# Kernel optimization log

Measured on AMD Instinct MI355X. Metric: run time of the kernel, lower is better.

The kernel has to match this reference:

```python
import jax, jax.numpy as jnp
import numpy as np

B, C, NUM_CLASSES = 16384, 4096, 64
BLOCK_LEN = 819          # round(4096 * 0.2)
N_BLOCKS = 1


def setup_inputs() -> dict:
    key = jax.random.key(0)
    kx, kw, ks = jax.random.split(key, 3)
    x = jax.random.normal(kx, (B, C), dtype=jnp.float32)
    W = jax.random.normal(kw, (NUM_CLASSES, C), dtype=jnp.float32) * 0.02
    b = jnp.zeros((NUM_CLASSES,), dtype=jnp.float32)
    # valid starts in [0, C - BLOCK_LEN], randint upper bound exclusive
    starts = jax.random.randint(ks, (B, N_BLOCKS), 0, C - BLOCK_LEN + 1, dtype=jnp.int32)
    return {"x": x, "W": W, "b": b, "starts": starts}


def reference(x, W, b, starts):
    # Vectorized DropBlock1D (training mode): zero a contiguous channel
    # segment of length BLOCK_LEN per sample per block, then Linear.
    pos = jnp.arange(C, dtype=jnp.int32)                      # [C]
    s = starts[:, :, None]                                    # [B, NB, 1]
    blocked = (pos[None, None, :] >= s) & (pos[None, None, :] < s + BLOCK_LEN)
    keep = ~jnp.any(blocked, axis=1)                           # [B, C]
    xm = x * keep.astype(x.dtype)                              # [B, C]
    return xm @ W.T + b                                        # [B, num_classes]
```

## Files before the change

### kernel.cpp

```cpp
#include <hip/hip_runtime.h>
#include <stdint.h>

#define BROWS 16384
#define CDIM  4096
#define NCLS  64
#define BLKLEN 819u
#define NWAVES 8
#define MROWS 32
#define CH 256
#define NCHUNK (CDIM / CH)

typedef __attribute__((ext_vector_type(4))) float f32x4;
typedef __attribute__((ext_vector_type(8))) short s16x8;

static __device__ __forceinline__ unsigned short f2bf(float f) {
    union { float f; unsigned u; } v; v.f = f;
    unsigned u = v.u;
    u += 0x7FFFu + ((u >> 16) & 1u);
    return (unsigned short)(u >> 16);
}

static __device__ __forceinline__ void gload_lds16(const void* g, void* l) {
    __builtin_amdgcn_global_load_lds(
        (const __attribute__((address_space(1))) unsigned int*)g,
        (__attribute__((address_space(3))) unsigned int*)l,
        16, 0, 0);
}

__global__ __launch_bounds__(256) void convert_w_fragmajor(const float* __restrict__ W,
                                                           unsigned short* __restrict__ Wfm) {
    const int u    = blockIdx.x * 256 + threadIdx.x;
    const int lane = u & 63;
    const int t    = (u >> 6) & 3;
    const int kk   = u >> 8;
    const int row  = t * 16 + (lane & 15);
    const int col  = kk * 32 + (lane >> 4) * 8;
    const float* p = W + (size_t)row * CDIM + col;
    f32x4 a = *reinterpret_cast<const f32x4*>(p);
    f32x4 b = *reinterpret_cast<const f32x4*>(p + 4);
    s16x8 o;
    #pragma unroll
    for (int j = 0; j < 4; ++j) {
        o[j]     = (short)f2bf(a[j]);
        o[j + 4] = (short)f2bf(b[j]);
    }
    *reinterpret_cast<s16x8*>(Wfm + (size_t)u * 8) = o;
}

template<bool PRECONV>
__global__ __launch_bounds__(512, 4) void dropblock_gemm_kernel(
    const float* __restrict__ x,
    const float* __restrict__ Wf,
    const unsigned short* __restrict__ Wfm,
    const float* __restrict__ bias,
    const int* __restrict__ starts,
    float* __restrict__ out)
{
    __shared__ float lds[NWAVES][2][MROWS][32];
    const int tid  = threadIdx.x;
    const int lane = tid & 63;
    const int wv   = tid >> 6;
    const int l16  = lane & 15;
    const int lg   = lane >> 4;
    const int row_base = blockIdx.x * MROWS;

    const int s0 = starts[row_base + l16];
    const int s1 = starts[row_base + 16 + l16];
    int sr[4];
    #pragma unroll
    for (int i = 0; i < 4; ++i) sr[i] = starts[row_base + i * 8 + (lane >> 3)];

    const unsigned swzA = (unsigned)((l16 & 7) << 4);
    char* mybuf = (char*)&lds[wv][0][0][0];

    f32x4 acc[2][4];
    #pragma unroll
    for (int f = 0; f < 2; ++f)
        #pragma unroll
        for (int t = 0; t < 4; ++t) acc[f][t] = (f32x4){0.f, 0.f, 0.f, 0.f};

    auto stage = [&](int ch, int b) {
        char* lb = mybuf + b * 4096;
        const size_t colbase = (size_t)ch * CH + (size_t)wv * 32;
        const char* gclamp = (const char*)x + ((size_t)row_base * CDIM + colbase) * 4;
        #pragma unroll
        for (int i = 0; i < 4; ++i) {
            const int r = i * 8 + (lane >> 3);
            const unsigned wb = ((unsigned)((lane & 7) * 16)) ^ ((unsigned)((r & 7) << 4));
            const int c0 = (int)colbase + (int)(wb >> 2);
            const bool fullmask = (unsigned)(c0 - sr[i]) <= (BLKLEN - 4u);
            const char* gnorm = (const char*)x
                + ((size_t)(row_base + r) * CDIM + colbase) * 4 + wb;
            const char* g = fullmask ? gclamp : gnorm;
            gload_lds16(g, lb + i * 1024);
        }
    };

    s16x8 wfr[2][4];
    auto loadW = [&](int ch, int b) {
        const int kk = ch * 8 + wv;
        #pragma unroll
        for (int t = 0; t < 4; ++t)
            wfr[b][t] = *reinterpret_cast<const s16x8*>(
                Wfm + ((size_t)((kk * 4 + t) * 64 + lane)) * 8);
    };

    stage(0, 0);
    if (PRECONV) loadW(0, 0);

    #pragma unroll
    for (int ch = 0; ch < NCHUNK; ++ch) {
        const int b = ch & 1;

        if (ch + 1 < NCHUNK) {
            if (PRECONV) loadW(ch + 1, b ^ 1);
            stage(ch + 1, b ^ 1);
        }

        __builtin_amdgcn_sched_barrier(0);
        if (ch + 1 < NCHUNK) {
            if (PRECONV) asm volatile("s_waitcnt vmcnt(8)" ::: "memory");
            else         asm volatile("s_waitcnt vmcnt(4)" ::: "memory");
        } else {
            asm volatile("s_waitcnt vmcnt(0)" ::: "memory");
        }
        __builtin_amdgcn_sched_barrier(0);

        const char* lb = mybuf + b * 4096;
        #pragma unroll
        for (int f = 0; f < 2; ++f) {
            const int row = f * 16 + l16;
            const unsigned a0 = (unsigned)(row * 128 + lg * 32);
            f32x4 xa = *reinterpret_cast<const f32x4*>(lb + (a0 ^ swzA));
            f32x4 xb = *reinterpret_cast<const f32x4*>(lb + ((a0 + 16) ^ swzA));

            const int d0 = ch * CH + wv * 32 + lg * 8 - (f ? s1 : s0);
            s16x8 afrag;
            #pragma unroll
            for (int j = 0; j < 4; ++j) {
                float va = ((unsigned)(d0 + j)     >= BLKLEN) ? xa[j] : 0.f;
                float vb = ((unsigned)(d0 + 4 + j) >= BLKLEN) ? xb[j] : 0.f;
                afrag[j]     = (short)f2bf(va);
                afrag[j + 4] = (short)f2bf(vb);
            }

            #pragma unroll
            for (int t = 0; t < 4; ++t) {
                s16x8 bfrag;
                if (PRECONV) {
                    bfrag = wfr[b][t];
                } else {
                    const int kk = ch * 8 + wv;
                    const float* wrow = Wf + (size_t)(t * 16 + l16) * CDIM + kk * 32 + lg * 8;
                    f32x4 wa = *reinterpret_cast<const f32x4*>(wrow);
                    f32x4 wb2 = *reinterpret_cast<const f32x4*>(wrow + 4);
                    #pragma unroll
                    for (int j = 0; j < 4; ++j) {
                        bfrag[j]     = (short)f2bf(wa[j]);
                        bfrag[j + 4] = (short)f2bf(wb2[j]);
                    }
                }
                acc[f][t] = __builtin_amdgcn_mfma_f32_16x16x32_bf16(afrag, bfrag, acc[f][t], 0, 0, 0);
            }
        }
    }

    float (*plds)[MROWS][64] = reinterpret_cast<float (*)[MROWS][64]>(&lds[0][0][0][0]);
    #pragma unroll
    for (int f = 0; f < 2; ++f)
        #pragma unroll
        for (int t = 0; t < 4; ++t)
            #pragma unroll
            for (int i = 0; i < 4; ++i)
                plds[wv][f * 16 + lg * 4 + i][t * 16 + l16] = acc[f][t][i];
    __syncthreads();

    const int row  = tid >> 4;
    const int col4 = (tid & 15) * 4;
    f32x4 sum = *reinterpret_cast<const f32x4*>(bias + col4);
    #pragma unroll
    for (int w = 0; w < NWAVES; ++w)
        sum += *reinterpret_cast<const f32x4*>(&plds[w][row][col4]);
    *reinterpret_cast<f32x4*>(out + (size_t)(row_base + row) * NCLS + col4) = sum;
}

extern "C" void kernel_launch(void* const* d_in, const int* in_sizes, int n_in,
                              void* d_out, int out_size, void* d_ws, size_t ws_size,
                              hipStream_t stream) {
    const float* x      = (const float*)d_in[0];
    const float* W      = (const float*)d_in[1];
    const float* b      = (const float*)d_in[2];
    const int*   starts = (const int*)d_in[3];
    float*       out    = (float*)d_out;

    const size_t wbytes = (size_t)NCLS * CDIM * sizeof(unsigned short);
    if (ws_size >= wbytes) {
        unsigned short* Wfm = (unsigned short*)d_ws;
        convert_w_fragmajor<<<128, 256, 0, stream>>>(W, Wfm);
        dropblock_gemm_kernel<true><<<BROWS / MROWS, 512, 0, stream>>>(x, W, Wfm, b, starts, out);
    } else {
        dropblock_gemm_kernel<false><<<BROWS / MROWS, 512, 0, stream>>>(x, W, nullptr, b, starts, out);
    }
}
```

Before: 49.84 us.

## Halve rows per block and deepen x staging to triple-buffered prefetch

Each block now handles 16 rows instead of 32, doubling the grid to 1024 blocks. Each wave keeps a single accumulator row-fragment. The per-wave LDS staging becomes a 3-deep ring so x chunks are prefetched two iterations ahead, with vmcnt waits adjusted to match. The aim is more parallelism and more latency hiding for this bandwidth-bound read of x. In exchange each W fragment is reused by half as many rows, so total W-fragment traffic doubles, and an extra barrier is added before the reduction.

```diff
diff --git a/kernel.cpp b/kernel.cpp
--- a/kernel.cpp
+++ b/kernel.cpp
@@ -6,11 +6,12 @@
 #define NCLS  64
 #define BLKLEN 819u
 #define NWAVES 8
-#define MROWS 32
+#define MROWS 16
 #define CH 256
 #define NCHUNK (CDIM / CH)
 
 typedef __attribute__((ext_vector_type(4))) float f32x4;
+typedef __attribute__((ext_vector_type(2))) float f32x2;
 typedef __attribute__((ext_vector_type(8))) short s16x8;
 
 static __device__ __forceinline__ unsigned short f2bf(float f) {
@@ -56,7 +57,7 @@
     const int* __restrict__ starts,
     float* __restrict__ out)
 {
-    __shared__ float lds[NWAVES][2][MROWS][32];
+    __shared__ float lds[NWAVES][3][MROWS][32];
     const int tid  = threadIdx.x;
     const int lane = tid & 63;
     const int wv   = tid >> 6;
@@ -65,26 +66,23 @@
     const int row_base = blockIdx.x * MROWS;
 
     const int s0 = starts[row_base + l16];
-    const int s1 = starts[row_base + 16 + l16];
-    int sr[4];
+    int sr[2];
     #pragma unroll
-    for (int i = 0; i < 4; ++i) sr[i] = starts[row_base + i * 8 + (lane >> 3)];
+    for (int i = 0; i < 2; ++i) sr[i] = starts[row_base + i * 8 + (lane >> 3)];
 
     const unsigned swzA = (unsigned)((l16 & 7) << 4);
     char* mybuf = (char*)&lds[wv][0][0][0];
 
-    f32x4 acc[2][4];
+    f32x4 acc[4];
     #pragma unroll
-    for (int f = 0; f < 2; ++f)
-        #pragma unroll
-        for (int t = 0; t < 4; ++t) acc[f][t] = (f32x4){0.f, 0.f, 0.f, 0.f};
+    for (int t = 0; t < 4; ++t) acc[t] = (f32x4){0.f, 0.f, 0.f, 0.f};
 
-    auto stage = [&](int ch, int b) {
-        char* lb = mybuf + b * 4096;
+    auto stage = [&](int ch, int bi) {
+        char* lb = mybuf + bi * 2048;
         const size_t colbase = (size_t)ch * CH + (size_t)wv * 32;
         const char* gclamp = (const char*)x + ((size_t)row_base * CDIM + colbase) * 4;
         #pragma unroll
-        for (int i = 0; i < 4; ++i) {
+        for (int i = 0; i < 2; ++i) {
             const int r = i * 8 + (lane >> 3);
             const unsigned wb = ((unsigned)((lane & 7) * 16)) ^ ((unsigned)((r & 7) << 4));
             const int c0 = (int)colbase + (int)(wb >> 2);
@@ -97,91 +95,87 @@
     };
 
     s16x8 wfr[2][4];
-    auto loadW = [&](int ch, int b) {
+    auto loadW = [&](int ch, int bi) {
         const int kk = ch * 8 + wv;
         #pragma unroll
         for (int t = 0; t < 4; ++t)
-            wfr[b][t] = *reinterpret_cast<const s16x8*>(
+            wfr[bi][t] = *reinterpret_cast<const s16x8*>(
                 Wfm + ((size_t)((kk * 4 + t) * 64 + lane)) * 8);
     };
 
     stage(0, 0);
     if (PRECONV) loadW(0, 0);
+    stage(1, 1);
 
     #pragma unroll
     for (int ch = 0; ch < NCHUNK; ++ch) {
-        const int b = ch & 1;
-
-        if (ch + 1 < NCHUNK) {
-            if (PRECONV) loadW(ch + 1, b ^ 1);
-            stage(ch + 1, b ^ 1);
-        }
+        if (PRECONV && ch + 1 < NCHUNK) loadW(ch + 1, (ch + 1) & 1);
+        if (ch + 2 < NCHUNK) stage(ch + 2, (ch + 2) % 3);
 
         __builtin_amdgcn_sched_barrier(0);
-        if (ch + 1 < NCHUNK) {
-            if (PRECONV) asm volatile("s_waitcnt vmcnt(8)" ::: "memory");
-            else         asm volatile("s_waitcnt vmcnt(4)" ::: "memory");
+        if (PRECONV) {
+            if (ch + 2 < NCHUNK)      asm volatile("s_waitcnt vmcnt(8)" ::: "memory");
+            else if (ch + 1 < NCHUNK) asm volatile("s_waitcnt vmcnt(6)" ::: "memory");
+            else                      asm volatile("s_waitcnt vmcnt(0)" ::: "memory");
         } else {
             asm volatile("s_waitcnt vmcnt(0)" ::: "memory");
         }
         __builtin_amdgcn_sched_barrier(0);
 
-        const char* lb = mybuf + b * 4096;
+        const char* lb = mybuf + (ch % 3) * 2048;
+        const unsigned a0 = (unsigned)(l16 * 128 + lg * 32);
+        f32x4 xa = *reinterpret_cast<const f32x4*>(lb + (a0 ^ swzA));
+        f32x4 xb = *reinterpret_cast<const f32x4*>(lb + ((a0 + 16) ^ swzA));
+
+        const int d0 = ch * CH + wv * 32 + lg * 8 - s0;
+        s16x8 afrag;
         #pragma unroll
-        for (int f = 0; f < 2; ++f) {
-            const int row = f * 16 + l16;
-            const unsigned a0 = (unsigned)(row * 128 + lg * 32);
-            f32x4 xa = *reinterpret_cast<const f32x4*>(lb + (a0 ^ swzA));
-            f32x4 xb = *reinterpret_cast<const f32x4*>(lb + ((a0 + 16) ^ swzA));
+        for (int j = 0; j < 4; ++j) {
+            float va = ((unsigned)(d0 + j)     >= BLKLEN) ? xa[j] : 0.f;
+            float vb = ((unsigned)(d0 + 4 + j) >= BLKLEN) ? xb[j] : 0.f;
+            afrag[j]     = (short)f2bf(va);
+            afrag[j + 4] = (short)f2bf(vb);
+        }
 
-            const int d0 = ch * CH + wv * 32 + lg * 8 - (f ? s1 : s0);
-            s16x8 afrag;
-            #pragma unroll
-            for (int j = 0; j < 4; ++j) {
-                float va = ((unsigned)(d0 + j)     >= BLKLEN) ? xa[j] : 0.f;
-                float vb = ((unsigned)(d0 + 4 + j) >= BLKLEN) ? xb[j] : 0.f;
-                afrag[j]     = (short)f2bf(va);
-                afrag[j + 4] = (short)f2bf(vb);
+        #pragma unroll
+        for (int t = 0; t < 4; ++t) {
+            s16x8 bfrag;
+            if (PRECONV) {
+                bfrag = wfr[ch & 1][t];
+            } else {
+                const int kk = ch * 8 + wv;
+                const float* wrow = Wf + (size_t)(t * 16 + l16) * CDIM + kk * 32 + lg * 8;
+                f32x4 wa = *reinterpret_cast<const f32x4*>(wrow);
+                f32x4 wb2 = *reinterpret_cast<const f32x4*>(wrow + 4);
+                #pragma unroll
+                for (int j = 0; j < 4; ++j) {
+                    bfrag[j]     = (short)f2bf(wa[j]);
+                    bfrag[j + 4] = (short)f2bf(wb2[j]);
+                }
             }
-
-            #pragma unroll
-            for (int t = 0; t < 4; ++t) {
-                s16x8 bfrag;
-                if (PRECONV) {
-                    bfrag = wfr[b][t];
-                } else {
-                    const int kk = ch * 8 + wv;
-                    const float* wrow = Wf + (size_t)(t * 16 + l16) * CDIM + kk * 32 + lg * 8;
-                    f32x4 wa = *reinterpret_cast<const f32x4*>(wrow);
-                    f32x4 wb2 = *reinterpret_cast<const f32x4*>(wrow + 4);
-                    #pragma unroll
-                    for (int j = 0; j < 4; ++j) {
-                        bfrag[j]     = (short)f2bf(wa[j]);
-                        bfrag[j + 4] = (short)f2bf(wb2[j]);
-                    }
-                }
-                acc[f][t] = __builtin_amdgcn_mfma_f32_16x16x32_bf16(afrag, bfrag, acc[f][t], 0, 0, 0);
-            }
+            acc[t] = __builtin_amdgcn_mfma_f32_16x16x32_bf16(afrag, bfrag, acc[t], 0, 0, 0);
         }
     }
 
+    __syncthreads();
     float (*plds)[MROWS][64] = reinterpret_cast<float (*)[MROWS][64]>(&lds[0][0][0][0]);
     #pragma unroll
-    for (int f = 0; f < 2; ++f)
+    for (int t = 0; t < 4; ++t)
         #pragma unroll
-        for (int t = 0; t < 4; ++t)
-            #pragma unroll
-            for (int i = 0; i < 4; ++i)
-                plds[wv][f * 16 + lg * 4 + i][t * 16 + l16] = acc[f][t][i];
+        for (int i = 0; i < 4; ++i)
+            plds[wv][lg * 4 + i][t * 16 + l16] = acc[t][i];
     __syncthreads();
 
-    const int row  = tid >> 4;
-    const int col4 = (tid & 15) * 4;
-    f32x4 sum = *reinterpret_cast<const f32x4*>(bias + col4);
+    const int row  = tid >> 5;
+    const int col2 = (tid & 31) * 2;
+    f32x2 sum = (f32x2){bias[col2], bias[col2 + 1]};
     #pragma unroll
-    for (int w = 0; w < NWAVES; ++w)
-        sum += *reinterpret_cast<const f32x4*>(&plds[w][row][col4]);
-    *reinterpret_cast<f32x4*>(out + (size_t)(row_base + row) * NCLS + col4) = sum;
+    for (int w = 0; w < NWAVES; ++w) {
+        f32x2 p = *reinterpret_cast<const f32x2*>(&plds[w][row][col2]);
+        sum[0] += p[0];
+        sum[1] += p[1];
+    }
+    *reinterpret_cast<f32x2*>(out + (size_t)(row_base + row) * NCLS + col2) = sum;
 }
 
 extern "C" void kernel_launch(void* const* d_in, const int* in_sizes, int n_in,
```

New measurement: 53.60 us. 7.5% more time.

## Split block waves by row half and K quarter instead of pure K split

Applied to the files above, without the earlier changes.

Each wave now handles 16 rows and 64 columns per chunk instead of 32 rows and 32 columns, so waves are arranged 2 (rows) x 4 (K). Each wave loads twice as many W fragments per chunk but does half the A conversion per row group. The final reduction sums 4 partials instead of 8. The staging swizzle and the waitcnt depth change to match. A __syncthreads is added before the partial-sum write into LDS, since the staging buffers are now shared across waves. This trades W register and bandwidth pressure for a cheaper cross-wave reduction and different x access patterns.

```diff
diff --git a/kernel.cpp b/kernel.cpp
--- a/kernel.cpp
+++ b/kernel.cpp
@@ -56,53 +56,55 @@
     const int* __restrict__ starts,
     float* __restrict__ out)
 {
-    __shared__ float lds[NWAVES][2][MROWS][32];
+    __shared__ float lds[NWAVES][2][16][64];
     const int tid  = threadIdx.x;
     const int lane = tid & 63;
     const int wv   = tid >> 6;
+    const int rh   = wv >> 2;
+    const int kq   = wv & 3;
     const int l16  = lane & 15;
     const int lg   = lane >> 4;
     const int row_base = blockIdx.x * MROWS;
-
-    const int s0 = starts[row_base + l16];
-    const int s1 = starts[row_base + 16 + l16];
+    const int wrb  = row_base + rh * 16;
+
+    const int s0 = starts[wrb + l16];
     int sr[4];
     #pragma unroll
-    for (int i = 0; i < 4; ++i) sr[i] = starts[row_base + i * 8 + (lane >> 3)];
-
-    const unsigned swzA = (unsigned)((l16 & 7) << 4);
+    for (int i = 0; i < 4; ++i) sr[i] = starts[wrb + i * 4 + lg];
+
     char* mybuf = (char*)&lds[wv][0][0][0];
 
-    f32x4 acc[2][4];
-    #pragma unroll
-    for (int f = 0; f < 2; ++f)
-        #pragma unroll
-        for (int t = 0; t < 4; ++t) acc[f][t] = (f32x4){0.f, 0.f, 0.f, 0.f};
+    f32x4 acc[4];
+    #pragma unroll
+    for (int t = 0; t < 4; ++t) acc[t] = (f32x4){0.f, 0.f, 0.f, 0.f};
 
     auto stage = [&](int ch, int b) {
         char* lb = mybuf + b * 4096;
-        const size_t colbase = (size_t)ch * CH + (size_t)wv * 32;
-        const char* gclamp = (const char*)x + ((size_t)row_base * CDIM + colbase) * 4;
+        const int colbase = ch * CH + kq * 64;
+        const char* gclamp = (const char*)x + ((size_t)wrb * CDIM + (size_t)colbase) * 4;
         #pragma unroll
         for (int i = 0; i < 4; ++i) {
-            const int r = i * 8 + (lane >> 3);
-            const unsigned wb = ((unsigned)((lane & 7) * 16)) ^ ((unsigned)((r & 7) << 4));
-            const int c0 = (int)colbase + (int)(wb >> 2);
+            const int r = i * 4 + lg;
+            const int q = (lane & 15) ^ r;
+            const int c0 = colbase + q * 4;
             const bool fullmask = (unsigned)(c0 - sr[i]) <= (BLKLEN - 4u);
             const char* gnorm = (const char*)x
-                + ((size_t)(row_base + r) * CDIM + colbase) * 4 + wb;
+                + ((size_t)(wrb + r) * CDIM + (size_t)colbase) * 4 + q * 16;
             const char* g = fullmask ? gclamp : gnorm;
             gload_lds16(g, lb + i * 1024);
         }
     };
 
-    s16x8 wfr[2][4];
+    s16x8 wfr[2][8];
     auto loadW = [&](int ch, int b) {
-        const int kk = ch * 8 + wv;
-        #pragma unroll
-        for (int t = 0; t < 4; ++t)
-            wfr[b][t] = *reinterpret_cast<const s16x8*>(
-                Wfm + ((size_t)((kk * 4 + t) * 64 + lane)) * 8);
+        #pragma unroll
+        for (int c = 0; c < 2; ++c) {
+            const int kk = ch * 8 + kq * 2 + c;
+            #pragma unroll
+            for (int t = 0; t < 4; ++t)
+                wfr[b][c * 4 + t] = *reinterpret_cast<const s16x8*>(
+                    Wfm + ((size_t)((kk * 4 + t) * 64 + lane)) * 8);
+        }
     };
 
     stage(0, 0);
@@ -119,22 +121,22 @@
 
         __builtin_amdgcn_sched_barrier(0);
         if (ch + 1 < NCHUNK) {
-            if (PRECONV) asm volatile("s_waitcnt vmcnt(8)" ::: "memory");
-            else         asm volatile("s_waitcnt vmcnt(4)" ::: "memory");
+            if (PRECONV) asm volatile("s_waitcnt vmcnt(12)" ::: "memory");
+            else         asm volatile("s_waitcnt vmcnt(4)"  ::: "memory");
         } else {
             asm volatile("s_waitcnt vmcnt(0)" ::: "memory");
         }
         __builtin_amdgcn_sched_barrier(0);
 
         const char* lb = mybuf + b * 4096;
-        #pragma unroll
-        for (int f = 0; f < 2; ++f) {
-            const int row = f * 16 + l16;
-            const unsigned a0 = (unsigned)(row * 128 + lg * 32);
-            f32x4 xa = *reinterpret_cast<const f32x4*>(lb + (a0 ^ swzA));
-            f32x4 xb = *reinterpret_cast<const f32x4*>(lb + ((a0 + 16) ^ swzA));
-
-            const int d0 = ch * CH + wv * 32 + lg * 8 - (f ? s1 : s0);
+        const unsigned swz = (unsigned)(l16 << 4);
+        #pragma unroll
+        for (int c = 0; c < 2; ++c) {
+            const unsigned a0 = (unsigned)(l16 * 256 + lg * 32 + c * 128);
+            f32x4 xa = *reinterpret_cast<const f32x4*>(lb + (a0 ^ swz));
+            f32x4 xb = *reinterpret_cast<const f32x4*>(lb + ((a0 + 16) ^ swz));
+
+            const int d0 = ch * CH + kq * 64 + c * 32 + lg * 8 - s0;
             s16x8 afrag;
             #pragma unroll
             for (int j = 0; j < 4; ++j) {
@@ -148,9 +150,9 @@
             for (int t = 0; t < 4; ++t) {
                 s16x8 bfrag;
                 if (PRECONV) {
-                    bfrag = wfr[b][t];
+                    bfrag = wfr[b][c * 4 + t];
                 } else {
-                    const int kk = ch * 8 + wv;
+                    const int kk = ch * 8 + kq * 2 + c;
                     const float* wrow = Wf + (size_t)(t * 16 + l16) * CDIM + kk * 32 + lg * 8;
                     f32x4 wa = *reinterpret_cast<const f32x4*>(wrow);
                     f32x4 wb2 = *reinterpret_cast<const f32x4*>(wrow + 4);
@@ -160,27 +162,27 @@
                         bfrag[j + 4] = (short)f2bf(wb2[j]);
                     }
                 }
-                acc[f][t] = __builtin_amdgcn_mfma_f32_16x16x32_bf16(afrag, bfrag, acc[f][t], 0, 0, 0);
+                acc[t] = __builtin_amdgcn_mfma_f32_16x16x32_bf16(afrag, bfrag, acc[t], 0, 0, 0);
             }
         }
     }
 
-    float (*plds)[MROWS][64] = reinterpret_cast<float (*)[MROWS][64]>(&lds[0][0][0][0]);
-    #pragma unroll
-    for (int f = 0; f < 2; ++f)
-        #pragma unroll
-        for (int t = 0; t < 4; ++t)
-            #pragma unroll
-            for (int i = 0; i < 4; ++i)
-                plds[wv][f * 16 + lg * 4 + i][t * 16 + l16] = acc[f][t][i];
+    __syncthreads();
+    float (*plds)[16][64] = reinterpret_cast<float (*)[16][64]>(&lds[0][0][0][0]);
+    #pragma unroll
+    for (int t = 0; t < 4; ++t)
+        #pragma unroll
+        for (int i = 0; i < 4; ++i)
+            plds[wv][lg * 4 + i][t * 16 + l16] = acc[t][i];
     __syncthreads();
 
     const int row  = tid >> 4;
     const int col4 = (tid & 15) * 4;
+    const int rh2  = row >> 4;
     f32x4 sum = *reinterpret_cast<const f32x4*>(bias + col4);
     #pragma unroll
-    for (int w = 0; w < NWAVES; ++w)
-        sum += *reinterpret_cast<const f32x4*>(&plds[w][row][col4]);
+    for (int q = 0; q < 4; ++q)
+        sum += *reinterpret_cast<const f32x4*>(&plds[rh2 * 4 + q][row & 15][col4]);
     *reinterpret_cast<f32x4*>(out + (size_t)(row_base + row) * NCLS + col4) = sum;
 }
 
```

After: 53.48 us. 1.07x slower.
